# Optimization experiments

Measured on AMD Instinct MI355X. Metric: run time of the kernel, lower is better.

## Reference

```python
import jax, jax.numpy as jnp
import numpy as np

D_MODEL = 2048
N_HEADS = 16
HEAD_DIM = D_MODEL // N_HEADS
B, T = 2, 2048


def setup_inputs() -> dict:
    key = jax.random.key(0)
    ks = jax.random.split(key, 7)
    s = 0.02
    return {
        "x": jax.random.normal(ks[0], (B, T, D_MODEL), dtype=jnp.float32),
        "w_qkv": jax.random.normal(ks[1], (D_MODEL, 3 * D_MODEL), dtype=jnp.float32) * s,
        "w_proj": jax.random.normal(ks[2], (D_MODEL, D_MODEL), dtype=jnp.float32) * s,
        "w_ff1": jax.random.normal(ks[3], (D_MODEL, 4 * D_MODEL), dtype=jnp.float32) * s,
        "b_ff1": jnp.zeros((4 * D_MODEL,), dtype=jnp.float32),
        "w_ff2": jax.random.normal(ks[4], (4 * D_MODEL, D_MODEL), dtype=jnp.float32) * s,
        "b_ff2": jnp.zeros((D_MODEL,), dtype=jnp.float32),
    }


def reference(x, w_qkv, w_proj, w_ff1, b_ff1, w_ff2, b_ff2):
    Bs, Ts, C = x.shape
    H, hd = N_HEADS, HEAD_DIM
    # fused qkv projection
    qkv = jnp.einsum("btc,cd->btd", x, w_qkv)
    q, k, v = jnp.split(qkv, 3, axis=-1)
    # (B, T, C) -> (B, H, T, hd)
    q = q.reshape(Bs, Ts, H, hd).transpose(0, 2, 1, 3)
    k = k.reshape(Bs, Ts, H, hd).transpose(0, 2, 1, 3)
    v = v.reshape(Bs, Ts, H, hd).transpose(0, 2, 1, 3)
    # paged KV write + gather round-trip (empty cache, n_kv_head == n_heads)
    # is the identity on k, v; attention is causal SDPA over the full cache.
    scale = 1.0 / jnp.sqrt(jnp.asarray(hd, dtype=x.dtype))
    scores = jnp.einsum("bhqd,bhkd->bhqk", q, k) * scale
    causal = jnp.tril(jnp.ones((Ts, Ts), dtype=bool))
    scores = jnp.where(causal, scores, jnp.finfo(scores.dtype).min)
    attn = jax.nn.softmax(scores, axis=-1)
    out = jnp.einsum("bhqk,bhkd->bhqd", attn, v)  # (B, H, T, hd)
    out = out.transpose(0, 2, 1, 3).reshape(Bs, Ts, C)
    attn_out = jnp.einsum("btc,cd->btd", out, w_proj)
    # feed-forward with exact GELU (torch nn.GELU default)
    h = jax.nn.gelu(jnp.einsum("btc,cf->btf", x, w_ff1) + b_ff1, approximate=False)
    ff_out = jnp.einsum("btf,fc->btc", h, w_ff2) + b_ff2
    return x + attn_out + ff_out
```

## Files before the change

kernel.cpp:

```cpp
#include <hip/hip_runtime.h>
#include <hip/hip_bf16.h>
#include <cmath>

typedef __bf16 bf16x8 __attribute__((ext_vector_type(8)));
typedef float f32x4 __attribute__((ext_vector_type(4)));
typedef unsigned short u16;
typedef unsigned int u32;

#define DEV __device__ __forceinline__

static constexpr int BB = 2;
static constexpr int T = 2048;
static constexpr int DM = 2048;
static constexpr int NH = 16;
static constexpr int HD = 128;
static constexpr int FF = 8192;
static constexpr int M = BB * T;
static constexpr int NQKV = 3 * DM;

DEV u16 f2b(float f) {
  u32 u = __builtin_bit_cast(u32, f);
  u = (u + 0x7FFFu + ((u >> 16) & 1u)) >> 16;
  return (u16)u;
}
DEV float b2f(u16 h) {
  u32 u = ((u32)h) << 16;
  return __builtin_bit_cast(float, u);
}

DEV void gload16(const u16* g, const u16* l) {
  __builtin_amdgcn_global_load_lds(
      (const __attribute__((address_space(1))) void*)(uintptr_t)g,
      (__attribute__((address_space(3))) void*)(unsigned)(uintptr_t)l,
      16, 0, 0);
}


__global__ void cvt_f32_to_bf16(const float* __restrict__ in, u16* __restrict__ out, int n4) {
  int i = blockIdx.x * blockDim.x + threadIdx.x;
  if (i >= n4) return;
  float4 v = reinterpret_cast<const float4*>(in)[i];
  ushort4 o;
  o.x = f2b(v.x); o.y = f2b(v.y); o.z = f2b(v.z); o.w = f2b(v.w);
  reinterpret_cast<ushort4*>(out)[i] = o;
}

__global__ void transpose_cvt(const float* __restrict__ W, u16* __restrict__ Wt, int K, int N) {
  __shared__ float tile[32][33];
  int nb = blockIdx.x * 32, kb = blockIdx.y * 32;
  int tx = threadIdx.x & 31, ty = threadIdx.x >> 5;
#pragma unroll
  for (int r = 0; r < 32; r += 8)
    tile[ty + r][tx] = W[(size_t)(kb + ty + r) * N + nb + tx];
  __syncthreads();
#pragma unroll
  for (int r = 0; r < 32; r += 8)
    Wt[(size_t)(nb + ty + r) * K + kb + tx] = f2b(tile[tx][ty + r]);
}

template <int EPI>
__global__ __launch_bounds__(256) void gemm_bf16(
    const u16* __restrict__ A, const u16* __restrict__ Bt, int Ndim, int K,
    u16* __restrict__ out_bf, float* __restrict__ out_f32,
    const float* __restrict__ bias,
    const float* __restrict__ resid_f32, const u16* __restrict__ resid_bf) {
  __shared__ __align__(16) u16 lds[3 * 2 * 128 * 32];
  const int t = threadIdx.x;
  const int m0 = blockIdx.y * 128, n0 = blockIdx.x * 128;
  const int wave = t >> 6, lane = t & 63;
  const int wm = wave >> 1, wn = wave & 1;
  const int lr = lane & 15, lk = lane >> 4;
  const int grow = wave * 16 + (lane >> 2);
  const int gk = (lane & 3) * 8;

  u16* cA = lds;                 u16* cB = lds + 4096;
  u16* nA = lds + 2 * 4096;      u16* nB = lds + 3 * 4096;
  u16* sA = lds + 4 * 4096;      u16* sB = lds + 5 * 4096;

  const u16* gA0 = &A[(size_t)(m0 + grow) * K + gk];
  const u16* gA1 = &A[(size_t)(m0 + 64 + grow) * K + gk];
  const u16* gB0 = &Bt[(size_t)(n0 + grow) * K + gk];
  const u16* gB1 = &Bt[(size_t)(n0 + 64 + grow) * K + gk];

  const int wb = wave * 16 * 32;

  auto stage = [&](u16* dA, u16* dB) {
    gload16(gA0, dA + wb);
    gload16(gA1, dA + 64 * 32 + wb);
    gload16(gB0, dB + wb);
    gload16(gB1, dB + 64 * 32 + wb);
    gA0 += 32; gA1 += 32; gB0 += 32; gB1 += 32;
  };

  const int NT = K >> 5;

  stage(cA, cB);
  stage(nA, nB);
  __builtin_amdgcn_sched_barrier(0);
  asm volatile("s_waitcnt vmcnt(4)" ::: "memory");
  __builtin_amdgcn_s_barrier();
  __builtin_amdgcn_sched_barrier(0);

  f32x4 acc[4][4] = {};

  for (int kt = 0; kt < NT; ++kt) {
    if (kt + 2 < NT) stage(sA, sB);
    bf16x8 af[4], bfr[4];
#pragma unroll
    for (int i = 0; i < 4; ++i) {
      af[i]  = *reinterpret_cast<const bf16x8*>(&cA[(wm * 64 + i * 16 + lr) * 32 + lk * 8]);
      bfr[i] = *reinterpret_cast<const bf16x8*>(&cB[(wn * 64 + i * 16 + lr) * 32 + lk * 8]);
    }
#pragma unroll
    for (int i = 0; i < 4; ++i)
#pragma unroll
      for (int j = 0; j < 4; ++j)
        acc[i][j] = __builtin_amdgcn_mfma_f32_16x16x32_bf16(af[i], bfr[j], acc[i][j], 0, 0, 0);
    if (kt + 1 < NT) {
      __builtin_amdgcn_sched_barrier(0);
      if (kt + 2 < NT) asm volatile("s_waitcnt vmcnt(4)" ::: "memory");
      else             asm volatile("s_waitcnt vmcnt(0)" ::: "memory");
      __builtin_amdgcn_s_barrier();
      __builtin_amdgcn_sched_barrier(0);
      u16* tA = cA; u16* tB = cB;
      cA = nA; cB = nB; nA = sA; nB = sB; sA = tA; sB = tB;
    }
  }

#pragma unroll
  for (int i = 0; i < 4; ++i) {
#pragma unroll
    for (int j = 0; j < 4; ++j) {
#pragma unroll
      for (int r = 0; r < 4; ++r) {
        int gr = m0 + wm * 64 + i * 16 + (lane >> 4) * 4 + r;
        int gc = n0 + wn * 64 + j * 16 + (lane & 15);
        float v = acc[i][j][r];
        if constexpr (EPI == 0) {
          int part = gc >> 11, cc = gc & 2047;
          int head = cc >> 7, d = cc & 127;
          int b = gr >> 11, tt = gr & 2047;
          out_bf[(size_t)part * M * DM + (((size_t)(b * NH + head) * T + tt) * HD + d)] = f2b(v);
        } else if constexpr (EPI == 1) {
          out_bf[(size_t)gr * Ndim + gc] = f2b(v);
        } else if constexpr (EPI == 2) {
          v += bias[gc];
          float u = v * (v * v * 0.044715f + 1.0f) * 0.7978845608028654f;
          float e = exp2f(u * 2.885390081777927f);
          float th = 1.0f - 2.0f / (e + 1.0f);
          v = 0.5f * v * (1.0f + th);
          out_bf[(size_t)gr * Ndim + gc] = f2b(v);
        } else if constexpr (EPI == 3) {
          v += bias[gc] + resid_f32[(size_t)gr * Ndim + gc] + b2f(resid_bf[(size_t)gr * Ndim + gc]);
          out_f32[(size_t)gr * Ndim + gc] = v;
        } else {
          int hh = gr >> 7, d = gr & 127;
          int b = gc >> 11, tt = gc & 2047;
          out_bf[((size_t)(b * NH + hh) * HD + d) * T + tt] = f2b(v);
        }
      }
    }
  }
}

__global__ __launch_bounds__(256) void attn_fwd(
    const u16* __restrict__ qg, const u16* __restrict__ kg,
    const u16* __restrict__ vt, u16* __restrict__ outg) {
  __shared__ __align__(16) u16 lK[64 * 128];
  __shared__ __align__(16) u16 lVt[128 * 64];
  __shared__ __align__(16) u16 lP[4][16 * 72];
  const int t = threadIdx.x;
  const int qi = blockIdx.x, bh = blockIdx.y;
  const int wv = t >> 6, lane = t & 63;
  const int lc = lane & 15, lg = lane >> 4;
  const size_t base = (size_t)bh * T * HD;
  const size_t vbase = (size_t)bh * HD * T;
  const int q0 = qi * 64;

  bf16x8 qf[4];
#pragma unroll
  for (int kk = 0; kk < 4; ++kk)
    qf[kk] = *reinterpret_cast<const bf16x8*>(
        &qg[base + (size_t)(q0 + wv * 16 + lc) * HD + kk * 32 + lg * 8]);

  f32x4 oacc[8] = {};
  float mrow[4], lrow[4];
#pragma unroll
  for (int r = 0; r < 4; ++r) { mrow[r] = -INFINITY; lrow[r] = 0.f; }

  const float scaleL = 0.08838834764831845f * 1.4426950408889634f;
  const int ntiles = qi + 1;
  for (int kt = 0; kt < ntiles; ++kt) {
    __syncthreads();
#pragma unroll
    for (int h = 0; h < 4; ++h) {
      int row = h * 16 + wv * 4 + (lane >> 4);
      int sb = ((lane & 15) * 16) ^ ((row & 7) << 4);
      gload16(&kg[base + (size_t)(kt * 64 + row) * HD + (sb >> 1)],
              (const u16*)((const char*)lK + (h * 256 + wv * 64) * 16));
    }
#pragma unroll
    for (int h = 0; h < 4; ++h) {
      int row = h * 32 + wv * 8 + (lane >> 3);
      int sb = ((lane & 7) * 16) ^ ((row & 7) << 4);
      gload16(&vt[vbase + (size_t)row * T + kt * 64 + (sb >> 1)],
              (const u16*)((const char*)lVt + (h * 256 + wv * 64) * 16));
    }
    __syncthreads();

    f32x4 s[4] = {};
#pragma unroll
    for (int nf = 0; nf < 4; ++nf) {
      int krow = nf * 16 + lc;
#pragma unroll
      for (int kk = 0; kk < 4; ++kk) {
        int dbyte = kk * 64 + lg * 16;
        bf16x8 kf = *reinterpret_cast<const bf16x8*>(
            reinterpret_cast<const char*>(lK) + krow * 256 + (dbyte ^ ((krow & 7) << 4)));
        s[nf] = __builtin_amdgcn_mfma_f32_16x16x32_bf16(qf[kk], kf, s[nf], 0, 0, 0);
      }
    }

    float rmax[4];
#pragma unroll
    for (int r = 0; r < 4; ++r) rmax[r] = -INFINITY;
#pragma unroll
    for (int nf = 0; nf < 4; ++nf) {
      int col = kt * 64 + nf * 16 + lc;
#pragma unroll
      for (int r = 0; r < 4; ++r) {
        int row = q0 + wv * 16 + lg * 4 + r;
        float sv = s[nf][r] * scaleL;
        if (col > row) sv = -INFINITY;
        s[nf][r] = sv;
        rmax[r] = fmaxf(rmax[r], sv);
      }
    }
#pragma unroll
    for (int mk = 1; mk < 16; mk <<= 1)
#pragma unroll
      for (int r = 0; r < 4; ++r)
        rmax[r] = fmaxf(rmax[r], __shfl_xor(rmax[r], mk));
    float corr[4];
#pragma unroll
    for (int r = 0; r < 4; ++r) {
      float mnew = fmaxf(mrow[r], rmax[r]);
      corr[r] = exp2f(mrow[r] - mnew);
      mrow[r] = mnew;
      lrow[r] *= corr[r];
    }
#pragma unroll
    for (int dc = 0; dc < 8; ++dc)
#pragma unroll
      for (int r = 0; r < 4; ++r) oacc[dc][r] *= corr[r];

#pragma unroll
    for (int nf = 0; nf < 4; ++nf) {
#pragma unroll
      for (int r = 0; r < 4; ++r) {
        float p = exp2f(s[nf][r] - mrow[r]);
        lrow[r] += p;
        lP[wv][(lg * 4 + r) * 72 + nf * 16 + lc] = f2b(p);
      }
    }
    bf16x8 pa[2];
#pragma unroll
    for (int kk = 0; kk < 2; ++kk)
      pa[kk] = *reinterpret_cast<const bf16x8*>(&lP[wv][lc * 72 + kk * 32 + lg * 8]);
#pragma unroll
    for (int dc = 0; dc < 8; ++dc) {
#pragma unroll
      for (int kk = 0; kk < 2; ++kk) {
        int vrow = dc * 16 + lc;
        int off = (kk * 64 + lg * 16) ^ ((vrow & 7) << 4);
        bf16x8 vf = *reinterpret_cast<const bf16x8*>(
            reinterpret_cast<const char*>(lVt) + vrow * 128 + off);
        oacc[dc] = __builtin_amdgcn_mfma_f32_16x16x32_bf16(pa[kk], vf, oacc[dc], 0, 0, 0);
      }
    }
  }

#pragma unroll
  for (int mk = 1; mk < 16; mk <<= 1)
#pragma unroll
    for (int r = 0; r < 4; ++r) lrow[r] += __shfl_xor(lrow[r], mk);

  const int b = bh >> 4, hh = bh & 15;
#pragma unroll
  for (int dc = 0; dc < 8; ++dc)
#pragma unroll
    for (int r = 0; r < 4; ++r) {
      int tt = q0 + wv * 16 + lg * 4 + r;
      int d = dc * 16 + lc;
      float o = oacc[dc][r] / lrow[r];
      outg[(size_t)(b * T + tt) * DM + hh * HD + d] = f2b(o);
    }
}


extern "C" void kernel_launch(void* const* d_in, const int* in_sizes, int n_in,
                              void* d_out, int out_size, void* d_ws, size_t ws_size,
                              hipStream_t stream) {
  const float* x      = (const float*)d_in[0];
  const float* w_qkv  = (const float*)d_in[1];
  const float* w_proj = (const float*)d_in[2];
  const float* w_ff1  = (const float*)d_in[3];
  const float* b_ff1  = (const float*)d_in[4];
  const float* w_ff2  = (const float*)d_in[5];
  const float* b_ff2  = (const float*)d_in[6];
  float* out = (float*)d_out;

  u16* ws = (u16*)d_ws;
  size_t o = 0;
  u16* x_bf      = ws + o; o += (size_t)M * DM;
  u16* wqkv_t    = ws + o; o += (size_t)NQKV * DM;
  u16* wproj_t   = ws + o; o += (size_t)DM * DM;
  u16* wff1_t    = ws + o; o += (size_t)FF * DM;
  u16* wff2_t    = ws + o; o += (size_t)DM * FF;
  u16* attn_proj = ws + o; o += (size_t)M * DM;
  u16* qbuf      = ws + o;
  u16* kbuf      = qbuf + (size_t)M * DM;
  u16* vtbuf     = kbuf + (size_t)M * DM;
  u16* attn_out  = vtbuf + (size_t)M * DM;
  u16* hbuf      = qbuf;

  cvt_f32_to_bf16<<<(M * DM / 4 + 255) / 256, 256, 0, stream>>>(x, x_bf, M * DM / 4);
  transpose_cvt<<<dim3(NQKV / 32, DM / 32), 256, 0, stream>>>(w_qkv, wqkv_t, DM, NQKV);
  transpose_cvt<<<dim3(DM / 32, DM / 32), 256, 0, stream>>>(w_proj, wproj_t, DM, DM);
  transpose_cvt<<<dim3(FF / 32, DM / 32), 256, 0, stream>>>(w_ff1, wff1_t, DM, FF);
  transpose_cvt<<<dim3(DM / 32, FF / 32), 256, 0, stream>>>(w_ff2, wff2_t, FF, DM);

  gemm_bf16<0><<<dim3(4096 / 128, M / 128), 256, 0, stream>>>(
      x_bf, wqkv_t, 4096, DM, qbuf, nullptr, nullptr, nullptr, nullptr);

  gemm_bf16<4><<<dim3(M / 128, DM / 128), 256, 0, stream>>>(
      wqkv_t + (size_t)4096 * DM, x_bf, M, DM, vtbuf, nullptr, nullptr, nullptr, nullptr);

  attn_fwd<<<dim3(T / 64, BB * NH), 256, 0, stream>>>(qbuf, kbuf, vtbuf, attn_out);

  gemm_bf16<1><<<dim3(DM / 128, M / 128), 256, 0, stream>>>(
      attn_out, wproj_t, DM, DM, attn_proj, nullptr, nullptr, nullptr, nullptr);

  gemm_bf16<2><<<dim3(FF / 128, M / 128), 256, 0, stream>>>(
      x_bf, wff1_t, FF, DM, hbuf, nullptr, b_ff1, nullptr, nullptr);

  gemm_bf16<3><<<dim3(DM / 128, M / 128), 256, 0, stream>>>(
      hbuf, wff2_t, DM, FF, nullptr, out, b_ff2, x, attn_proj);
}
```

Baseline: 730.1 us.

## Enlarge GEMM tiles to 256x128 with XCD swizzle, reverse attention order, lazy rescale

The GEMM moves to 512-thread blocks with 256x128 tiles. A 1D grid is remapped so consecutive tiles land on the same XCD, which should improve operand reuse and L2 locality. The attention kernel now launches the longest causal query blocks first to balance the tail, and it skips the online-softmax rescale unless the running max grows by more than a threshold. The lazy rescale relies on fp32 headroom, and the larger tile needs more LDS per block, which may reduce occupancy.

After: 691.1 us. 1.06x faster.

```diff
diff --git a/kernel.cpp b/kernel.cpp
--- a/kernel.cpp
+++ b/kernel.cpp
@@ -59,37 +59,35 @@
 }
 
 template <int EPI>
-__global__ __launch_bounds__(256) void gemm_bf16(
-    const u16* __restrict__ A, const u16* __restrict__ Bt, int Ndim, int K,
+__global__ __launch_bounds__(512, 4) void gemm_bf16(
+    const u16* __restrict__ A, const u16* __restrict__ Bt, int Ndim, int K, int gx,
     u16* __restrict__ out_bf, float* __restrict__ out_f32,
     const float* __restrict__ bias,
     const float* __restrict__ resid_f32, const u16* __restrict__ resid_bf) {
-  __shared__ __align__(16) u16 lds[3 * 2 * 128 * 32];
+  __shared__ __align__(16) u16 lds[3 * (256 + 128) * 32];
   const int t = threadIdx.x;
-  const int m0 = blockIdx.y * 128, n0 = blockIdx.x * 128;
+  const int nwg = gridDim.x, cpx = nwg >> 3;
+  const int wg = (blockIdx.x & 7) * cpx + (blockIdx.x >> 3);
+  const int m0 = (wg / gx) * 256, n0 = (wg % gx) * 128;
   const int wave = t >> 6, lane = t & 63;
   const int wm = wave >> 1, wn = wave & 1;
   const int lr = lane & 15, lk = lane >> 4;
-  const int grow = wave * 16 + (lane >> 2);
-  const int gk = (lane & 3) * 8;
-
-  u16* cA = lds;                 u16* cB = lds + 4096;
-  u16* nA = lds + 2 * 4096;      u16* nB = lds + 3 * 4096;
-  u16* sA = lds + 4 * 4096;      u16* sB = lds + 5 * 4096;
-
-  const u16* gA0 = &A[(size_t)(m0 + grow) * K + gk];
-  const u16* gA1 = &A[(size_t)(m0 + 64 + grow) * K + gk];
-  const u16* gB0 = &Bt[(size_t)(n0 + grow) * K + gk];
-  const u16* gB1 = &Bt[(size_t)(n0 + 64 + grow) * K + gk];
-
-  const int wb = wave * 16 * 32;
+
+  u16* cA = lds;                   u16* cB = lds + 8192;
+  u16* nA = lds + 12288;           u16* nB = lds + 12288 + 8192;
+  u16* sA = lds + 2 * 12288;       u16* sB = lds + 2 * 12288 + 8192;
+
+  const u16* gA0 = &A[(size_t)(m0 + wave * 16 + (lane >> 2)) * K + (lane & 3) * 8];
+  const u16* gA1 = gA0 + (size_t)128 * K;
+  const u16* gB0 = &Bt[(size_t)(n0 + wave * 16 + (lane >> 2)) * K + (lane & 3) * 8];
+
+  const int wbase = wave * 512;
 
   auto stage = [&](u16* dA, u16* dB) {
-    gload16(gA0, dA + wb);
-    gload16(gA1, dA + 64 * 32 + wb);
-    gload16(gB0, dB + wb);
-    gload16(gB1, dB + 64 * 32 + wb);
-    gA0 += 32; gA1 += 32; gB0 += 32; gB1 += 32;
+    gload16(gA0, dA + wbase);
+    gload16(gA1, dA + 4096 + wbase);
+    gload16(gB0, dB + wbase);
+    gA0 += 32; gA1 += 32; gB0 += 32;
   };
 
   const int NT = K >> 5;
@@ -97,7 +95,7 @@
   stage(cA, cB);
   stage(nA, nB);
   __builtin_amdgcn_sched_barrier(0);
-  asm volatile("s_waitcnt vmcnt(4)" ::: "memory");
+  asm volatile("s_waitcnt vmcnt(3)" ::: "memory");
   __builtin_amdgcn_s_barrier();
   __builtin_amdgcn_sched_barrier(0);
 
@@ -118,7 +116,7 @@
         acc[i][j] = __builtin_amdgcn_mfma_f32_16x16x32_bf16(af[i], bfr[j], acc[i][j], 0, 0, 0);
     if (kt + 1 < NT) {
       __builtin_amdgcn_sched_barrier(0);
-      if (kt + 2 < NT) asm volatile("s_waitcnt vmcnt(4)" ::: "memory");
+      if (kt + 2 < NT) asm volatile("s_waitcnt vmcnt(3)" ::: "memory");
       else             asm volatile("s_waitcnt vmcnt(0)" ::: "memory");
       __builtin_amdgcn_s_barrier();
       __builtin_amdgcn_sched_barrier(0);
@@ -170,7 +168,8 @@
   __shared__ __align__(16) u16 lVt[128 * 64];
   __shared__ __align__(16) u16 lP[4][16 * 72];
   const int t = threadIdx.x;
-  const int qi = blockIdx.x, bh = blockIdx.y;
+  const int qi = gridDim.x - 1 - blockIdx.x;
+  const int bh = blockIdx.y;
   const int wv = t >> 6, lane = t & 63;
   const int lc = lane & 15, lg = lane >> 4;
   const size_t base = (size_t)bh * T * HD;
@@ -241,18 +240,24 @@
 #pragma unroll
       for (int r = 0; r < 4; ++r)
         rmax[r] = fmaxf(rmax[r], __shfl_xor(rmax[r], mk));
-    float corr[4];
-#pragma unroll
-    for (int r = 0; r < 4; ++r) {
-      float mnew = fmaxf(mrow[r], rmax[r]);
-      corr[r] = exp2f(mrow[r] - mnew);
-      mrow[r] = mnew;
-      lrow[r] *= corr[r];
-    }
-#pragma unroll
-    for (int dc = 0; dc < 8; ++dc)
-#pragma unroll
-      for (int r = 0; r < 4; ++r) oacc[dc][r] *= corr[r];
+
+    int need = 0;
+#pragma unroll
+    for (int r = 0; r < 4; ++r) need |= (rmax[r] > mrow[r] + 11.5f) ? 1 : 0;
+    if (__any(need)) {
+      float corr[4];
+#pragma unroll
+      for (int r = 0; r < 4; ++r) {
+        float mnew = fmaxf(mrow[r], rmax[r]);
+        corr[r] = exp2f(mrow[r] - mnew);
+        mrow[r] = mnew;
+        lrow[r] *= corr[r];
+      }
+#pragma unroll
+      for (int dc = 0; dc < 8; ++dc)
+#pragma unroll
+        for (int r = 0; r < 4; ++r) oacc[dc][r] *= corr[r];
+    }
 
 #pragma unroll
     for (int nf = 0; nf < 4; ++nf) {
@@ -330,20 +335,20 @@
   transpose_cvt<<<dim3(FF / 32, DM / 32), 256, 0, stream>>>(w_ff1, wff1_t, DM, FF);
   transpose_cvt<<<dim3(DM / 32, FF / 32), 256, 0, stream>>>(w_ff2, wff2_t, FF, DM);
 
-  gemm_bf16<0><<<dim3(4096 / 128, M / 128), 256, 0, stream>>>(
-      x_bf, wqkv_t, 4096, DM, qbuf, nullptr, nullptr, nullptr, nullptr);
-
-  gemm_bf16<4><<<dim3(M / 128, DM / 128), 256, 0, stream>>>(
-      wqkv_t + (size_t)4096 * DM, x_bf, M, DM, vtbuf, nullptr, nullptr, nullptr, nullptr);
+  gemm_bf16<0><<<512, 512, 0, stream>>>(
+      x_bf, wqkv_t, 4096, DM, 32, qbuf, nullptr, nullptr, nullptr, nullptr);
+
+  gemm_bf16<4><<<256, 512, 0, stream>>>(
+      wqkv_t + (size_t)4096 * DM, x_bf, M, DM, 32, vtbuf, nullptr, nullptr, nullptr, nullptr);
 
   attn_fwd<<<dim3(T / 64, BB * NH), 256, 0, stream>>>(qbuf, kbuf, vtbuf, attn_out);
 
-  gemm_bf16<1><<<dim3(DM / 128, M / 128), 256, 0, stream>>>(
-      attn_out, wproj_t, DM, DM, attn_proj, nullptr, nullptr, nullptr, nullptr);
-
-  gemm_bf16<2><<<dim3(FF / 128, M / 128), 256, 0, stream>>>(
-      x_bf, wff1_t, FF, DM, hbuf, nullptr, b_ff1, nullptr, nullptr);
-
-  gemm_bf16<3><<<dim3(DM / 128, M / 128), 256, 0, stream>>>(
-      hbuf, wff2_t, DM, FF, nullptr, out, b_ff2, x, attn_proj);
-}
+  gemm_bf16<1><<<256, 512, 0, stream>>>(
+      attn_out, wproj_t, DM, DM, 16, attn_proj, nullptr, nullptr, nullptr, nullptr);
+
+  gemm_bf16<2><<<1024, 512, 0, stream>>>(
+      x_bf, wff1_t, FF, DM, 64, hbuf, nullptr, b_ff1, nullptr, nullptr);
+
+  gemm_bf16<3><<<256, 512, 0, stream>>>(
+      hbuf, wff2_t, DM, FF, 16, nullptr, out, b_ff2, x, attn_proj);
+}
```
